# Kernel tuning notes

Measured on AMD Instinct MI355X. Metric: run time of the kernel, lower is better.

## Reference

```python
import jax, jax.numpy as jnp
import numpy as np

EMB_SZ = 1024
NUM_HEADS = 16
HEAD_SIZE = EMB_SZ // NUM_HEADS  # 64; inputs must have last dim == HEAD_SIZE (module quirk)
B, S = 2, 2048


def setup_inputs() -> dict:
    key = jax.random.key(0)
    ks = jax.random.split(key, 8)
    return {
        "inputs_for_keys": jax.random.normal(ks[0], (B, S, HEAD_SIZE), jnp.float32),
        "inputs_for_values": jax.random.normal(ks[1], (B, S, HEAD_SIZE), jnp.float32),
        "inputs_for_queries": jax.random.normal(ks[2], (B, S, HEAD_SIZE), jnp.float32),
        # per-head projection weights, stacked over heads (glorot-ish scale)
        "Wk": jax.random.normal(ks[3], (NUM_HEADS, HEAD_SIZE, HEAD_SIZE), jnp.float32) * 0.125,
        "Wv": jax.random.normal(ks[4], (NUM_HEADS, HEAD_SIZE, HEAD_SIZE), jnp.float32) * 0.125,
        "Wq": jax.random.normal(ks[5], (NUM_HEADS, HEAD_SIZE, HEAD_SIZE), jnp.float32) * 0.125,
        "Wo": jax.random.normal(ks[6], (EMB_SZ, EMB_SZ), jnp.float32) * 0.03,
        "bo": jnp.zeros((EMB_SZ,), jnp.float32),
    }


def reference(inputs_for_keys, inputs_for_values, inputs_for_queries, Wk, Wv, Wq, Wo, bo):
    # Each head sees the SAME full inputs (module quirk), distinct weights per head.
    K = jnp.einsum('bsd,hde->bhse', inputs_for_keys, Wk)      # [B,H,Sk,hs]
    V = jnp.einsum('bsd,hde->bhse', inputs_for_values, Wv)    # [B,H,Sk,hs]
    Q = jnp.einsum('bsd,hde->bhse', inputs_for_queries, Wq)   # [B,H,Sq,hs]

    Sq, Sk = Q.shape[2], K.shape[2]
    scores = jnp.einsum('bhqe,bhke->bhqk', Q, K)              # [B,H,Sq,Sk]
    # causal additive mask: -inf strictly above the diagonal (as in np.triu(..., k=1))
    mask = jnp.triu(jnp.full((Sq, Sk), -jnp.inf, dtype=scores.dtype), k=1)
    scale = jnp.asarray(Sk, scores.dtype) ** 0.5
    # NOTE: original divides AFTER adding the mask; -inf/scale == -inf so math matches
    attn = jax.nn.softmax((scores + mask) / scale, axis=-1)   # [B,H,Sq,Sk]

    heads = jnp.einsum('bhqk,bhke->bhqe', attn, V)            # [B,H,Sq,hs]
    # concat heads along last dim (head order matches the Python-loop concat)
    concat = heads.transpose(0, 2, 1, 3).reshape(heads.shape[0], Sq, -1)  # [B,Sq,emb]
    return concat @ Wo + bo                                   # Dense(emb_sz), linear activation
```

## Files before the change

### kernel.cpp

```cpp
#include <hip/hip_runtime.h>
#include <hip/hip_bf16.h>
#include <cstdint>

typedef unsigned short u16;
typedef __bf16 bf16x8 __attribute__((ext_vector_type(8)));
typedef u16 u16x8 __attribute__((ext_vector_type(8)));
typedef unsigned u32x4 __attribute__((ext_vector_type(4)));
typedef float f32x2 __attribute__((ext_vector_type(2)));
typedef float f32x4 __attribute__((ext_vector_type(4)));
typedef float f32x16 __attribute__((ext_vector_type(16)));

#define B_ 2
#define S_ 2048
#define H_ 16
#define HS_ 64
#define EMB_ 1024
#define QSCALE 0.022097086912079608f
#define LOG2E  1.4426950408889634f

static __device__ __forceinline__ u16 f2bf(float f) {
  unsigned int u = __float_as_uint(f);
  u += 0x7fffu + ((u >> 16) & 1u);
  return (u16)(u >> 16);
}

static __device__ __forceinline__ float ex2(float x) {
#if __has_builtin(__builtin_amdgcn_exp2f)
  return __builtin_amdgcn_exp2f(x);
#else
  float r; asm("v_exp_f32 %0, %1" : "=v"(r) : "v"(x)); return r;
#endif
}

static __device__ __forceinline__ float tsum16(const f32x16& s) {
  float a0 = s[0] + s[1],  a1 = s[2] + s[3];
  float a2 = s[4] + s[5],  a3 = s[6] + s[7];
  float a4 = s[8] + s[9],  a5 = s[10] + s[11];
  float a6 = s[12] + s[13], a7 = s[14] + s[15];
  a0 += a1; a2 += a3; a4 += a5; a6 += a7;
  a0 += a2; a4 += a6;
  return a0 + a4;
}

static __device__ __forceinline__ f32x4 mfma16(u16x8 a, u16x8 b, f32x4 c) {
  return __builtin_amdgcn_mfma_f32_16x16x32_bf16(
      __builtin_bit_cast(bf16x8, a), __builtin_bit_cast(bf16x8, b), c, 0, 0, 0);
}
static __device__ __forceinline__ f32x16 mfma32(u16x8 a, u16x8 b, f32x16 c) {
  return __builtin_amdgcn_mfma_f32_32x32x16_bf16(
      __builtin_bit_cast(bf16x8, a), __builtin_bit_cast(bf16x8, b), c, 0, 0, 0);
}

static __device__ __forceinline__ char* swzb(void* base, int row, int colbyte) {
  return (char*)base + ((row * 128 + colbyte) ^ ((row & 7) << 4));
}
static __device__ __forceinline__ u16x8* swzp(void* base, int row, int colbyte) {
  return (u16x8*)swzb(base, row, colbyte);
}

static __device__ __forceinline__ void pk_swap(float a0, float a1, float b0, float b1,
                                               unsigned& x, unsigned& y) {
  unsigned A, Bv;
  asm("v_cvt_pk_bf16_f32 %0, %1, %2" : "=v"(A) : "v"(a0), "v"(a1));
  asm("v_cvt_pk_bf16_f32 %0, %1, %2" : "=v"(Bv) : "v"(b0), "v"(b1));
  asm("v_permlane32_swap_b32 %0, %1" : "+v"(A), "+v"(Bv));
  x = A; y = Bv;
}

static __device__ __forceinline__ void pack2(const f32x16& s0, u16x8& pf0, u16x8& pf1) {
  unsigned w0, w1, w2, w3;
  pk_swap(s0[0], s0[1], s0[4], s0[5], w0, w2);
  pk_swap(s0[2], s0[3], s0[6], s0[7], w1, w3);
  pf0 = __builtin_bit_cast(u16x8, (u32x4){w0, w1, w2, w3});
  pk_swap(s0[8], s0[9], s0[12], s0[13], w0, w2);
  pk_swap(s0[10], s0[11], s0[14], s0[15], w1, w3);
  pf1 = __builtin_bit_cast(u16x8, (u32x4){w0, w1, w2, w3});
}

__global__ __launch_bounds__(256) void k_transpose_wo(const float* __restrict__ Wo,
                                                      u16* __restrict__ Wot) {
  __shared__ __align__(16) u16 T[64][72];
  const int kb = blockIdx.y * 64, nb = blockIdx.x * 64;
  const int r = threadIdx.x >> 2;
  const int c0 = (threadIdx.x & 3) << 4;
  const float* src = Wo + (size_t)(kb + r) * EMB_ + nb + c0;
#pragma unroll
  for (int i = 0; i < 16; i += 4) {
    float4 f = *(const float4*)(src + i);
    T[c0 + i + 0][r] = f2bf(f.x);
    T[c0 + i + 1][r] = f2bf(f.y);
    T[c0 + i + 2][r] = f2bf(f.z);
    T[c0 + i + 3][r] = f2bf(f.w);
  }
  __syncthreads();
  u16* dst = Wot + (size_t)(nb + r) * EMB_ + kb + c0;
  *(u16x8*)(dst)     = *(const u16x8*)&T[r][c0];
  *(u16x8*)(dst + 8) = *(const u16x8*)&T[r][c0 + 8];
}

__global__ __launch_bounds__(256) void k_proj(
    const float* __restrict__ xq, const float* __restrict__ xk, const float* __restrict__ xv,
    const float* __restrict__ Wq, const float* __restrict__ Wk, const float* __restrict__ Wv,
    u16* __restrict__ Qf, u16* __restrict__ Kf, u16* __restrict__ Vf) {
  __shared__ __align__(16) u16 Xb[64][64];
  __shared__ __align__(16) u16 Wb[64][64];
  __shared__ __align__(16) u16 Tt[64][64];
  const int sb = blockIdx.x;
  const int bh = blockIdx.y;
  const int tn = blockIdx.z;
  const int b = bh >> 4, h = bh & 15;
  const int t = threadIdx.x;
  const int r = t >> 2, c0 = (t & 3) << 4;
  const int lane = t & 63, wv = t >> 6;
  const int lq = lane & 15, lg = lane >> 4;
  const int l31 = lane & 31, hi = lane >> 5;
  const float* xs = (tn == 0) ? xq : (tn == 1) ? xk : xv;
  const float* wsp3 = (tn == 0) ? Wq : (tn == 1) ? Wk : Wv;

  const float* src = xs + ((size_t)(b * S_ + sb * 64 + r)) * HS_ + c0;
#pragma unroll
  for (int i = 0; i < 16; i += 8) {
    float4 fa = *(const float4*)(src + i);
    float4 fb = *(const float4*)(src + i + 4);
    u16x8 v = {f2bf(fa.x), f2bf(fa.y), f2bf(fa.z), f2bf(fa.w),
               f2bf(fb.x), f2bf(fb.y), f2bf(fb.z), f2bf(fb.w)};
    *swzp(Xb, r, (c0 + i) * 2) = v;
  }
  const float* wsp = wsp3 + ((size_t)(h * HS_ + r)) * HS_ + c0;
#pragma unroll
  for (int i = 0; i < 16; i += 4) {
    float4 f = *(const float4*)(wsp + i);
    *(u16*)swzb(Wb, c0 + i + 0, r * 2) = f2bf(f.x);
    *(u16*)swzb(Wb, c0 + i + 1, r * 2) = f2bf(f.y);
    *(u16*)swzb(Wb, c0 + i + 2, r * 2) = f2bf(f.z);
    *(u16*)swzb(Wb, c0 + i + 3, r * 2) = f2bf(f.w);
  }
  __syncthreads();
  if (tn < 2) {
    u16x8 a0 = *swzp(Xb, wv * 16 + lq, lg * 16);
    u16x8 a1 = *swzp(Xb, wv * 16 + lq, 64 + lg * 16);
    const float osc = (tn == 0) ? (QSCALE * LOG2E) : 1.0f;
#pragma unroll
    for (int et = 0; et < 4; ++et) {
      u16x8 b0 = *swzp(Wb, et * 16 + lq, lg * 16);
      u16x8 b1 = *swzp(Wb, et * 16 + lq, 64 + lg * 16);
      f32x4 acc = {0.f, 0.f, 0.f, 0.f};
      acc = mfma16(a0, b0, acc);
      acc = mfma16(a1, b1, acc);
#pragma unroll
      for (int rr = 0; rr < 4; ++rr)
        *(u16*)swzb(Tt, wv * 16 + lg * 4 + rr, (et * 16 + lq) * 2) = f2bf(acc[rr] * osc);
    }
  } else {
    u16x8 xb0 = *swzp(Xb, wv * 16 + lq, lg * 16);
    u16x8 xb1 = *swzp(Xb, wv * 16 + lq, 64 + lg * 16);
#pragma unroll
    for (int et = 0; et < 4; ++et) {
      u16x8 a0 = *swzp(Wb, et * 16 + lq, lg * 16);
      u16x8 a1 = *swzp(Wb, et * 16 + lq, 64 + lg * 16);
      f32x4 acc = {0.f, 0.f, 0.f, 0.f};
      acc = mfma16(a0, xb0, acc);
      acc = mfma16(a1, xb1, acc);
#pragma unroll
      for (int rr = 0; rr < 4; ++rr)
        *(u16*)swzb(Tt, et * 16 + lg * 4 + rr, (wv * 16 + lq) * 2) = f2bf(acc[rr]);
    }
  }
  __syncthreads();
  if (tn < 2) {
    u16* dst = (tn == 0) ? Qf : Kf;
#pragma unroll
    for (int tl = 0; tl < 2; ++tl) {
      u16x8 v = *swzp(Tt, tl * 32 + l31, wv * 32 + hi * 16);
      size_t off = (((size_t)(bh * 64 + sb * 2 + tl)) * 4 + wv) * 512 + lane * 8;
      *(u16x8*)(dst + off) = v;
    }
  } else {
#pragma unroll
    for (int eta = 0; eta < 2; ++eta) {
      u16x8 v = *swzp(Tt, eta * 32 + l31, wv * 32 + hi * 16);
      size_t off = ((((size_t)(bh * 32 + sb)) * 2 + eta) * 4 + wv) * 512 + lane * 8;
      *(u16x8*)(Vf + off) = v;
    }
  }
}

__global__ __launch_bounds__(256, 2) void k_attn(
    const u16* __restrict__ Qf, const u16* __restrict__ Kf, const u16* __restrict__ Vf,
    u16* __restrict__ Co) {
  __shared__ float Xch[3][64][66];
  __shared__ __align__(16) u16 OswE[32][64];
  __shared__ __align__(16) u16 OswO[32][64];
  const int bid = blockIdx.x;
  const int xcd = bid & 7, idx = bid >> 3;
  const int bh = (xcd << 2) | (idx & 3);
  const int p = idx >> 2;
  const int b = bh >> 4, h = bh & 15;
  const int w = threadIdx.x >> 6;
  const int l = threadIdx.x & 63;
  const int lq = l & 31, hi = l >> 5;
  const float NEG = -3.0e38f;

  const u16* Kbase = Kf + ((size_t)(bh * 64) * 4) * 512 + l * 8;
  const u16* Vbase = Vf + ((size_t)(bh * 32) * 8) * 512 + l * 8;

#pragma unroll 1
  for (int ph = 0; ph < 2; ++ph) {
    const int g = ph ? (31 - p) : p;
    const int n = g + 1;
    const int js = (w * n) >> 2;
    const int je = ((w + 1) * n) >> 2;
    const bool dw = (w == 3);
    const int t32s = 2 * js;
    const int t32e = dw ? 2 * (n - 1) : 2 * je;
    const int tlim = dw ? t32e + 1 : t32e;

    const u16* Qe = Qf + (((size_t)(bh * 64 + 2 * g)) * 4) * 512 + l * 8;
    u16x8 qfe[4], qfo[4];
#pragma unroll
    for (int ss = 0; ss < 4; ++ss) {
      qfe[ss] = *(const u16x8*)(Qe + ss * 512);
      qfo[ss] = *(const u16x8*)(Qe + (4 + ss) * 512);
    }

    f32x16 o0e, o1e, o0o, o1o;
#pragma unroll
    for (int r = 0; r < 16; ++r) { o0e[r] = 0.f; o1e[r] = 0.f; o0o[r] = 0.f; o1o[r] = 0.f; }
    float lle = 0.f, llo = 0.f;

    u16x8 kf4[4], vf4[4];
    const bool havework = dw || (js < je);
    if (havework) {
      const u16* pk = Kbase + ((size_t)t32s * 4) * 512;
      size_t vb = ((size_t)(t32s >> 1) * 8 + (size_t)(t32s & 1) * 2);
#pragma unroll
      for (int ss = 0; ss < 4; ++ss) kf4[ss] = *(const u16x8*)(pk + ss * 512);
      vf4[0] = *(const u16x8*)(Vbase + (vb + 0) * 512);
      vf4[1] = *(const u16x8*)(Vbase + (vb + 1) * 512);
      vf4[2] = *(const u16x8*)(Vbase + (vb + 4) * 512);
      vf4[3] = *(const u16x8*)(Vbase + (vb + 5) * 512);
    }

    for (int t32 = t32s; t32 < t32e; ++t32) {
      const bool pre = (t32 + 1 < tlim);
      u16x8 pfA, pfB;
      f32x16 s;
#pragma unroll
      for (int r = 0; r < 16; ++r) s[r] = -16.f;
      __builtin_amdgcn_s_setprio(1);
      s = mfma32(kf4[0], qfe[0], s);
      s = mfma32(kf4[1], qfe[1], s);
      s = mfma32(kf4[2], qfe[2], s);
      s = mfma32(kf4[3], qfe[3], s);
      __builtin_amdgcn_s_setprio(0);
#pragma unroll
      for (int r = 0; r < 16; ++r) s[r] = ex2(s[r]);
      lle += tsum16(s);
      pack2(s, pfA, pfB);
      __builtin_amdgcn_s_setprio(1);
      o0e = mfma32(vf4[0], pfA, o0e);
      o0e = mfma32(vf4[1], pfB, o0e);
      o1e = mfma32(vf4[2], pfA, o1e);
      o1e = mfma32(vf4[3], pfB, o1e);
      __builtin_amdgcn_s_setprio(0);
#pragma unroll
      for (int r = 0; r < 16; ++r) s[r] = -16.f;
      __builtin_amdgcn_s_setprio(1);
      s = mfma32(kf4[0], qfo[0], s);
      s = mfma32(kf4[1], qfo[1], s);
      s = mfma32(kf4[2], qfo[2], s);
      s = mfma32(kf4[3], qfo[3], s);
      __builtin_amdgcn_s_setprio(0);
      if (pre) {
        const u16* pk = Kbase + ((size_t)(t32 + 1) * 4) * 512;
#pragma unroll
        for (int ss = 0; ss < 4; ++ss) kf4[ss] = *(const u16x8*)(pk + ss * 512);
      }
#pragma unroll
      for (int r = 0; r < 16; ++r) s[r] = ex2(s[r]);
      llo += tsum16(s);
      pack2(s, pfA, pfB);
      __builtin_amdgcn_s_setprio(1);
      o0o = mfma32(vf4[0], pfA, o0o);
      o0o = mfma32(vf4[1], pfB, o0o);
      o1o = mfma32(vf4[2], pfA, o1o);
      o1o = mfma32(vf4[3], pfB, o1o);
      __builtin_amdgcn_s_setprio(0);
      if (pre) {
        size_t vb = ((size_t)((t32 + 1) >> 1) * 8 + (size_t)((t32 + 1) & 1) * 2);
        vf4[0] = *(const u16x8*)(Vbase + (vb + 0) * 512);
        vf4[1] = *(const u16x8*)(Vbase + (vb + 1) * 512);
        vf4[2] = *(const u16x8*)(Vbase + (vb + 4) * 512);
        vf4[3] = *(const u16x8*)(Vbase + (vb + 5) * 512);
      }
    }

    if (dw) {
      u16x8 kf2[4], vf2[4];
      {
        const int t1 = 2 * n - 1;
        const u16* pk = Kbase + ((size_t)t1 * 4) * 512;
        size_t vb = ((size_t)(t1 >> 1) * 8 + (size_t)(t1 & 1) * 2);
#pragma unroll
        for (int ss = 0; ss < 4; ++ss) kf2[ss] = *(const u16x8*)(pk + ss * 512);
        vf2[0] = *(const u16x8*)(Vbase + (vb + 0) * 512);
        vf2[1] = *(const u16x8*)(Vbase + (vb + 1) * 512);
        vf2[2] = *(const u16x8*)(Vbase + (vb + 4) * 512);
        vf2[3] = *(const u16x8*)(Vbase + (vb + 5) * 512);
      }
      u16x8 pfA, pfB;
      f32x16 s;
#pragma unroll
      for (int r = 0; r < 16; ++r) s[r] = -16.f;
      s = mfma32(kf4[0], qfe[0], s);
      s = mfma32(kf4[1], qfe[1], s);
      s = mfma32(kf4[2], qfe[2], s);
      s = mfma32(kf4[3], qfe[3], s);
#pragma unroll
      for (int r = 0; r < 16; ++r) {
        int crow = (r & 3) + 8 * (r >> 2) + 4 * hi;
        if (crow > lq) s[r] = NEG;
      }
#pragma unroll
      for (int r = 0; r < 16; ++r) s[r] = ex2(s[r]);
      lle += tsum16(s);
      pack2(s, pfA, pfB);
      o0e = mfma32(vf4[0], pfA, o0e);
      o0e = mfma32(vf4[1], pfB, o0e);
      o1e = mfma32(vf4[2], pfA, o1e);
      o1e = mfma32(vf4[3], pfB, o1e);
#pragma unroll
      for (int r = 0; r < 16; ++r) s[r] = -16.f;
      s = mfma32(kf4[0], qfo[0], s);
      s = mfma32(kf4[1], qfo[1], s);
      s = mfma32(kf4[2], qfo[2], s);
      s = mfma32(kf4[3], qfo[3], s);
#pragma unroll
      for (int r = 0; r < 16; ++r) s[r] = ex2(s[r]);
      llo += tsum16(s);
      pack2(s, pfA, pfB);
      o0o = mfma32(vf4[0], pfA, o0o);
      o0o = mfma32(vf4[1], pfB, o0o);
      o1o = mfma32(vf4[2], pfA, o1o);
      o1o = mfma32(vf4[3], pfB, o1o);
#pragma unroll
      for (int r = 0; r < 16; ++r) s[r] = -16.f;
      s = mfma32(kf2[0], qfo[0], s);
      s = mfma32(kf2[1], qfo[1], s);
      s = mfma32(kf2[2], qfo[2], s);
      s = mfma32(kf2[3], qfo[3], s);
#pragma unroll
      for (int r = 0; r < 16; ++r) {
        int crow = (r & 3) + 8 * (r >> 2) + 4 * hi;
        if (crow > lq) s[r] = NEG;
      }
#pragma unroll
      for (int r = 0; r < 16; ++r) s[r] = ex2(s[r]);
      llo += tsum16(s);
      pack2(s, pfA, pfB);
      o0o = mfma32(vf2[0], pfA, o0o);
      o0o = mfma32(vf2[1], pfB, o0o);
      o1o = mfma32(vf2[2], pfA, o1o);
      o1o = mfma32(vf2[3], pfB, o1o);
    }

    if (w) {
      f32x2* xr = (f32x2*)(&Xch[w - 1][l][0]);
#pragma unroll
      for (int i = 0; i < 8; ++i) {
        xr[i]      = (f32x2){o0e[2 * i], o0e[2 * i + 1]};
        xr[8 + i]  = (f32x2){o1e[2 * i], o1e[2 * i + 1]};
        xr[16 + i] = (f32x2){o0o[2 * i], o0o[2 * i + 1]};
        xr[24 + i] = (f32x2){o1o[2 * i], o1o[2 * i + 1]};
      }
      xr[32] = (f32x2){lle, llo};
    }
    __syncthreads();
    if (w == 0) {
#pragma unroll
      for (int wv = 0; wv < 3; ++wv) {
        const f32x2* xr = (const f32x2*)(&Xch[wv][l][0]);
#pragma unroll
        for (int i = 0; i < 8; ++i) {
          f32x2 a = xr[i], bq = xr[8 + i], c = xr[16 + i], d = xr[24 + i];
          o0e[2 * i] += a[0]; o0e[2 * i + 1] += a[1];
          o1e[2 * i] += bq[0]; o1e[2 * i + 1] += bq[1];
          o0o[2 * i] += c[0]; o0o[2 * i + 1] += c[1];
          o1o[2 * i] += d[0]; o1o[2 * i + 1] += d[1];
        }
        f32x2 e = xr[32];
        lle += e[0]; llo += e[1];
      }
      lle += __shfl_xor(lle, 32);
      llo += __shfl_xor(llo, 32);
      {
        float inv = 1.0f / lle;
#pragma unroll
        for (int r = 0; r < 16; ++r) {
          int drow = (r & 3) + 8 * (r >> 2) + 4 * hi;
          *(u16*)swzb(OswE, lq, drow * 2) = f2bf(o0e[r] * inv);
          *(u16*)swzb(OswE, lq, (32 + drow) * 2) = f2bf(o1e[r] * inv);
        }
        u16* dst = Co + ((size_t)(b * S_ + 64 * g + lq)) * EMB_ + h * HS_ + hi * 32;
#pragma unroll
        for (int k = 0; k < 4; ++k) {
          u16x8 vv = *swzp(OswE, lq, (hi * 32 + k * 8) * 2);
          *(u16x8*)(dst + k * 8) = vv;
        }
      }
      {
        float inv = 1.0f / llo;
#pragma unroll
        for (int r = 0; r < 16; ++r) {
          int drow = (r & 3) + 8 * (r >> 2) + 4 * hi;
          *(u16*)swzb(OswO, lq, drow * 2) = f2bf(o0o[r] * inv);
          *(u16*)swzb(OswO, lq, (32 + drow) * 2) = f2bf(o1o[r] * inv);
        }
        u16* dst = Co + ((size_t)(b * S_ + 64 * g + 32 + lq)) * EMB_ + h * HS_ + hi * 32;
#pragma unroll
        for (int k = 0; k < 4; ++k) {
          u16x8 vv = *swzp(OswO, lq, (hi * 32 + k * 8) * 2);
          *(u16x8*)(dst + k * 8) = vv;
        }
      }
    }
    __syncthreads();
  }
}

__global__ __launch_bounds__(256) void k_outproj(
    const u16* __restrict__ Cc, const u16* __restrict__ Wot,
    const float* __restrict__ bo, float* __restrict__ out) {
  __shared__ __align__(16) u16 As[64][64];
  __shared__ __align__(16) u16 Bs[128][64];
  const int bid = blockIdx.x;
  const int xcd = bid & 7, sl = bid >> 3;
  const int mb = (xcd << 3) | (sl >> 3);
  const int nb = sl & 7;
  const int t = threadIdx.x;
  const int lane = t & 63, wv = t >> 6;
  const int lq = lane & 15, lg = lane >> 4;
  const int wr = wv >> 1, wc = wv & 1;
  const int lrow = lane >> 3;
  const int lchk = ((lane & 7) ^ (lane >> 3)) * 8;
  f32x4 acc[2][4];
#pragma unroll
  for (int mi = 0; mi < 2; ++mi)
#pragma unroll
    for (int ni = 0; ni < 4; ++ni) { f32x4 z = {0.f, 0.f, 0.f, 0.f}; acc[mi][ni] = z; }
  const u16* ga0 = Cc + (size_t)(mb * 64 + wv * 16 + lrow) * EMB_ + lchk;
  const u16* ga1 = Cc + (size_t)(mb * 64 + wv * 16 + 8 + lrow) * EMB_ + lchk;
  const u16* gb0 = Wot + (size_t)(nb * 128 + wv * 32 + lrow) * EMB_ + lchk;
  const u16* gb1 = Wot + (size_t)(nb * 128 + wv * 32 + 8 + lrow) * EMB_ + lchk;
  const u16* gb2 = Wot + (size_t)(nb * 128 + wv * 32 + 16 + lrow) * EMB_ + lchk;
  const u16* gb3 = Wot + (size_t)(nb * 128 + wv * 32 + 24 + lrow) * EMB_ + lchk;
  typedef __attribute__((address_space(3))) void lds_v;
  typedef const __attribute__((address_space(1))) void glb_v;
  for (int kt = 0; kt < 16; ++kt) {
    __syncthreads();
    const int co = kt * 64;
    __builtin_amdgcn_global_load_lds((glb_v*)(ga0 + co), (lds_v*)&As[wv * 16][0], 16, 0, 0);
    __builtin_amdgcn_global_load_lds((glb_v*)(ga1 + co), (lds_v*)&As[wv * 16 + 8][0], 16, 0, 0);
    __builtin_amdgcn_global_load_lds((glb_v*)(gb0 + co), (lds_v*)&Bs[wv * 32][0], 16, 0, 0);
    __builtin_amdgcn_global_load_lds((glb_v*)(gb1 + co), (lds_v*)&Bs[wv * 32 + 8][0], 16, 0, 0);
    __builtin_amdgcn_global_load_lds((glb_v*)(gb2 + co), (lds_v*)&Bs[wv * 32 + 16][0], 16, 0, 0);
    __builtin_amdgcn_global_load_lds((glb_v*)(gb3 + co), (lds_v*)&Bs[wv * 32 + 24][0], 16, 0, 0);
    __syncthreads();
#pragma unroll
    for (int kf = 0; kf < 2; ++kf) {
      u16x8 af[2], bf[4];
#pragma unroll
      for (int mi = 0; mi < 2; ++mi)
        af[mi] = *swzp(As, wr * 32 + mi * 16 + lq, kf * 64 + lg * 16);
#pragma unroll
      for (int ni = 0; ni < 4; ++ni)
        bf[ni] = *swzp(Bs, wc * 64 + ni * 16 + lq, kf * 64 + lg * 16);
#pragma unroll
      for (int mi = 0; mi < 2; ++mi)
#pragma unroll
        for (int ni = 0; ni < 4; ++ni)
          acc[mi][ni] = mfma16(af[mi], bf[ni], acc[mi][ni]);
    }
  }
#pragma unroll
  for (int mi = 0; mi < 2; ++mi) {
#pragma unroll
    for (int ni = 0; ni < 4; ++ni) {
      int col = nb * 128 + wc * 64 + ni * 16 + lq;
      float bv = bo[col];
#pragma unroll
      for (int rr = 0; rr < 4; ++rr) {
        int row = mb * 64 + wr * 32 + mi * 16 + lg * 4 + rr;
        out[(size_t)row * EMB_ + col] = acc[mi][ni][rr] + bv;
      }
    }
  }
}

extern "C" void kernel_launch(void* const* d_in, const int* in_sizes, int n_in,
                              void* d_out, int out_size, void* d_ws, size_t ws_size,
                              hipStream_t stream) {
  const float* xk = (const float*)d_in[0];
  const float* xv = (const float*)d_in[1];
  const float* xq = (const float*)d_in[2];
  const float* Wk = (const float*)d_in[3];
  const float* Wv = (const float*)d_in[4];
  const float* Wq = (const float*)d_in[5];
  const float* Wo = (const float*)d_in[6];
  const float* bo = (const float*)d_in[7];
  float* out = (float*)d_out;
  char* ws = (char*)d_ws;
  const size_t MB8 = (size_t)8 * 1024 * 1024;
  u16* Qfw = (u16*)(ws);
  u16* Kfw = (u16*)(ws + MB8);
  u16* Vfw = (u16*)(ws + 2 * MB8);
  u16* Cw  = (u16*)(ws + 3 * MB8);
  u16* Wot = (u16*)(ws + 4 * MB8);

  k_transpose_wo<<<dim3(16, 16), 256, 0, stream>>>(Wo, Wot);
  k_proj<<<dim3(32, 32, 3), 256, 0, stream>>>(xq, xk, xv, Wq, Wk, Wv, Qfw, Kfw, Vfw);
  k_attn<<<512, 256, 0, stream>>>(Qfw, Kfw, Vfw, Cw);
  k_outproj<<<512, 256, 0, stream>>>(Cw, Wot, bo, out);
}
```

Before: 64.84 us.

## Tree-reduce cross-wave partials and reuse fragment registers in diagonal block

The cross-wave reduction of attention partials now runs as a two-level tree (waves 1,3 into 0,2, then 2 into 0) instead of wave 0 serially summing three buffers, shrinking the LDS exchange buffer from three slots to two. The diagonal-block path drops the separate kf2/vf2 fragment arrays and reloads the next K/V fragments into the existing kf4/vf4 registers after their last use. This lowers register and LDS pressure, which could raise occupancy. The cost is two extra block barriers and loads that sit closer to their consumers, with less latency hiding.

```diff
diff --git a/kernel.cpp b/kernel.cpp
--- a/kernel.cpp
+++ b/kernel.cpp
@@ -188,7 +188,7 @@
 __global__ __launch_bounds__(256, 2) void k_attn(
     const u16* __restrict__ Qf, const u16* __restrict__ Kf, const u16* __restrict__ Vf,
     u16* __restrict__ Co) {
-  __shared__ float Xch[3][64][66];
+  __shared__ float Xch[2][64][66];
   __shared__ __align__(16) u16 OswE[32][64];
   __shared__ __align__(16) u16 OswO[32][64];
   const int bid = blockIdx.x;
@@ -296,18 +296,6 @@
     }
 
     if (dw) {
-      u16x8 kf2[4], vf2[4];
-      {
-        const int t1 = 2 * n - 1;
-        const u16* pk = Kbase + ((size_t)t1 * 4) * 512;
-        size_t vb = ((size_t)(t1 >> 1) * 8 + (size_t)(t1 & 1) * 2);
-#pragma unroll
-        for (int ss = 0; ss < 4; ++ss) kf2[ss] = *(const u16x8*)(pk + ss * 512);
-        vf2[0] = *(const u16x8*)(Vbase + (vb + 0) * 512);
-        vf2[1] = *(const u16x8*)(Vbase + (vb + 1) * 512);
-        vf2[2] = *(const u16x8*)(Vbase + (vb + 4) * 512);
-        vf2[3] = *(const u16x8*)(Vbase + (vb + 5) * 512);
-      }
       u16x8 pfA, pfB;
       f32x16 s;
 #pragma unroll
@@ -335,6 +323,12 @@
       s = mfma32(kf4[1], qfo[1], s);
       s = mfma32(kf4[2], qfo[2], s);
       s = mfma32(kf4[3], qfo[3], s);
+      {
+        const int t1 = 2 * n - 1;
+        const u16* pk = Kbase + ((size_t)t1 * 4) * 512;
+#pragma unroll
+        for (int ss = 0; ss < 4; ++ss) kf4[ss] = *(const u16x8*)(pk + ss * 512);
+      }
 #pragma unroll
       for (int r = 0; r < 16; ++r) s[r] = ex2(s[r]);
       llo += tsum16(s);
@@ -343,12 +337,20 @@
       o0o = mfma32(vf4[1], pfB, o0o);
       o1o = mfma32(vf4[2], pfA, o1o);
       o1o = mfma32(vf4[3], pfB, o1o);
+      {
+        const int t1 = 2 * n - 1;
+        size_t vb = ((size_t)(t1 >> 1) * 8 + (size_t)(t1 & 1) * 2);
+        vf4[0] = *(const u16x8*)(Vbase + (vb + 0) * 512);
+        vf4[1] = *(const u16x8*)(Vbase + (vb + 1) * 512);
+        vf4[2] = *(const u16x8*)(Vbase + (vb + 4) * 512);
+        vf4[3] = *(const u16x8*)(Vbase + (vb + 5) * 512);
+      }
 #pragma unroll
       for (int r = 0; r < 16; ++r) s[r] = -16.f;
-      s = mfma32(kf2[0], qfo[0], s);
-      s = mfma32(kf2[1], qfo[1], s);
-      s = mfma32(kf2[2], qfo[2], s);
-      s = mfma32(kf2[3], qfo[3], s);
+      s = mfma32(kf4[0], qfo[0], s);
+      s = mfma32(kf4[1], qfo[1], s);
+      s = mfma32(kf4[2], qfo[2], s);
+      s = mfma32(kf4[3], qfo[3], s);
 #pragma unroll
       for (int r = 0; r < 16; ++r) {
         int crow = (r & 3) + 8 * (r >> 2) + 4 * hi;
@@ -358,14 +360,14 @@
       for (int r = 0; r < 16; ++r) s[r] = ex2(s[r]);
       llo += tsum16(s);
       pack2(s, pfA, pfB);
-      o0o = mfma32(vf2[0], pfA, o0o);
-      o0o = mfma32(vf2[1], pfB, o0o);
-      o1o = mfma32(vf2[2], pfA, o1o);
-      o1o = mfma32(vf2[3], pfB, o1o);
-    }
-
-    if (w) {
-      f32x2* xr = (f32x2*)(&Xch[w - 1][l][0]);
+      o0o = mfma32(vf4[0], pfA, o0o);
+      o0o = mfma32(vf4[1], pfB, o0o);
+      o1o = mfma32(vf4[2], pfA, o1o);
+      o1o = mfma32(vf4[3], pfB, o1o);
+    }
+
+    if (w == 1 || w == 3) {
+      f32x2* xr = (f32x2*)(&Xch[w >> 1][l][0]);
 #pragma unroll
       for (int i = 0; i < 8; ++i) {
         xr[i]      = (f32x2){o0e[2 * i], o0e[2 * i + 1]};
@@ -376,10 +378,35 @@
       xr[32] = (f32x2){lle, llo};
     }
     __syncthreads();
+    if (w == 0 || w == 2) {
+      const f32x2* xr = (const f32x2*)(&Xch[w >> 1][l][0]);
+#pragma unroll
+      for (int i = 0; i < 8; ++i) {
+        f32x2 a = xr[i], bq = xr[8 + i], c = xr[16 + i], d = xr[24 + i];
+        o0e[2 * i] += a[0]; o0e[2 * i + 1] += a[1];
+        o1e[2 * i] += bq[0]; o1e[2 * i + 1] += bq[1];
+        o0o[2 * i] += c[0]; o0o[2 * i + 1] += c[1];
+        o1o[2 * i] += d[0]; o1o[2 * i + 1] += d[1];
+      }
+      f32x2 e = xr[32];
+      lle += e[0]; llo += e[1];
+    }
+    __syncthreads();
+    if (w == 2) {
+      f32x2* xr = (f32x2*)(&Xch[0][l][0]);
+#pragma unroll
+      for (int i = 0; i < 8; ++i) {
+        xr[i]      = (f32x2){o0e[2 * i], o0e[2 * i + 1]};
+        xr[8 + i]  = (f32x2){o1e[2 * i], o1e[2 * i + 1]};
+        xr[16 + i] = (f32x2){o0o[2 * i], o0o[2 * i + 1]};
+        xr[24 + i] = (f32x2){o1o[2 * i], o1o[2 * i + 1]};
+      }
+      xr[32] = (f32x2){lle, llo};
+    }
+    __syncthreads();
     if (w == 0) {
-#pragma unroll
-      for (int wv = 0; wv < 3; ++wv) {
-        const f32x2* xr = (const f32x2*)(&Xch[wv][l][0]);
+      {
+        const f32x2* xr = (const f32x2*)(&Xch[0][l][0]);
 #pragma unroll
         for (int i = 0; i < 8; ++i) {
           f32x2 a = xr[i], bq = xr[8 + i], c = xr[16 + i], d = xr[24 + i];
```

Measured after the change: 62.53 us. 1.04x faster.
